# Kernel tuning notes

Hardware: AMD Instinct MI355X
Metric: run time of the kernel (lower is better)

Reference implementation:

```python
import jax, jax.numpy as jnp
import numpy as np

N_U, N_I, D_IN_U, D_IN_I, D, D_QOL, B = 4096, 4096, 256, 256, 256, 4, 8192

def _w(key, shape, scale=0.05):
    return (jax.random.normal(key, shape) * scale).astype(jnp.float32)

def setup_inputs() -> dict:
    key = jax.random.key(0)
    ks = jax.random.split(key, 24)
    inp = {
        "x_u": jax.random.normal(ks[0], (N_U, D_IN_U), jnp.float32),
        "x_i": jax.random.normal(ks[1], (N_I, D_IN_I), jnp.float32),
        "social_adj": jax.random.randint(ks[2], (N_U, N_U), 0, 2, jnp.int32),
        "ui_adj": jax.random.randint(ks[3], (N_U, N_I), 0, 2, jnp.int32),
        "user_idx": jax.random.randint(ks[4], (B,), 0, N_U, jnp.int32),
        "item_idx": jax.random.randint(ks[5], (B,), 0, N_I, jnp.int32),
        "q_u": jax.random.normal(ks[6], (N_U, D_QOL), jnp.float32),
        # params (Linear stored as [in, out]; y = x @ W + b)
        "user_W": _w(ks[7], (D_IN_U, D)), "user_b": jnp.zeros((D,), jnp.float32),
        "item_W": _w(ks[8], (D_IN_I, D)), "item_b": jnp.zeros((D,), jnp.float32),
        "soc_W": _w(ks[9], (D, D)), "soc_a": _w(ks[10], (2 * D,)),
        "cnt_W": _w(ks[11], (D, D)), "cnt_a": _w(ks[12], (2 * D,)),
        "gate_W": _w(ks[13], (D_QOL, D)), "gate_b": jnp.zeros((D,), jnp.float32),
        "qproj_W": _w(ks[14], (D_QOL, D)), "qproj_b": jnp.zeros((D,), jnp.float32),
        "alpha_q": jnp.float32(0.3),
        "pred_W1": _w(ks[15], (2 * D, D)), "pred_b1": jnp.zeros((D,), jnp.float32),
        "pred_W2": _w(ks[16], (D, 1)), "pred_b2": jnp.zeros((1,), jnp.float32),
    }
    return inp

def _gat(Wh_src, Wh_dst, a, adj):
    """GAT additive attention: src rows attend over dst cols where adj!=0.
    Rows with no neighbors produce zero output (matches nan_to_num + zeroing)."""
    d = Wh_src.shape[-1]
    a1 = Wh_src @ a[:d]          # [N_src]
    a2 = Wh_dst @ a[d:]          # [N_dst]
    e = jax.nn.leaky_relu(a1[:, None] + a2[None, :], 0.2)  # [N_src, N_dst]
    mask = adj != 0
    neg_inf = jnp.float32(-jnp.inf)
    m = jnp.max(jnp.where(mask, e, neg_inf), axis=-1, keepdims=True)
    m = jnp.where(jnp.isfinite(m), m, 0.0)  # guard empty rows
    ex = jnp.where(mask, jnp.exp(e - m), 0.0)
    denom = jnp.sum(ex, axis=-1, keepdims=True)
    alpha = jnp.where(denom > 0, ex / jnp.where(denom > 0, denom, 1.0), 0.0)
    out = alpha @ Wh_dst
    return out, alpha

def reference(x_u, x_i, social_adj, ui_adj, user_idx, item_idx, q_u,
              user_W, user_b, item_W, item_b, soc_W, soc_a, cnt_W, cnt_a,
              gate_W, gate_b, qproj_W, qproj_b, alpha_q,
              pred_W1, pred_b1, pred_W2, pred_b2):
    h_u = x_u @ user_W + user_b               # [N_u, D]
    h_i = x_i @ item_W + item_b               # [N_i, D]
    # social attention (users over users)
    Wh = h_u @ soc_W
    soc_msg, alpha_s = _gat(Wh, Wh, soc_a, social_adj)
    # content attention (users over items)
    Wu = h_u @ cnt_W
    Wi = h_i @ cnt_W
    cnt_msg, alpha_c = _gat(Wu, Wi, cnt_a, ui_adj)
    h_u_out = jax.nn.elu(soc_msg + cnt_msg + h_u)
    # QoL gate
    gate = jax.nn.sigmoid(q_u @ gate_W + gate_b)
    qproj = q_u @ qproj_W + qproj_b
    h_u_out = h_u_out + alpha_q * gate * qproj
    # pair prediction (dropout inactive at eval)
    cat = jnp.concatenate([h_u_out[user_idx], h_i[item_idx]], axis=-1)  # [B, 2D]
    hid = jax.nn.relu(cat @ pred_W1 + pred_b1)
    r = (hid @ pred_W2 + pred_b2)[..., 0]
    r_hat = 1.0 + 4.0 * jax.nn.sigmoid(r)
    return r_hat, alpha_s, alpha_c
```

## Files before the change

### kernel.cpp

```cpp
#include <hip/hip_runtime.h>

typedef unsigned short u16;
typedef unsigned int u32;
typedef unsigned char u8;
typedef unsigned long long u64;
typedef float f32x4 __attribute__((ext_vector_type(4)));
typedef __bf16 bf16x8 __attribute__((ext_vector_type(8)));

#define NU 4096
#define DD 256
#define BB 8192

__device__ inline u16 f2b(float f) {
    u32 u = __builtin_bit_cast(u32, f);
    u32 r = (u + 0x7fffu + ((u >> 16) & 1u)) >> 16;
    return (u16)r;
}
__device__ inline float b2f(u16 v) { return __builtin_bit_cast(float, (u32)v << 16); }
__device__ inline float lrelu(float x) { return x > 0.f ? x : 0.2f * x; }
__device__ inline float decmax(u32 e) {
    return __builtin_bit_cast(float, (e >> 31) ? (e & 0x7fffffffu) : ~e);
}

#define BARRIER_LGKM() asm volatile("s_waitcnt lgkmcnt(0)\ns_barrier" ::: "memory")

__global__ __launch_bounds__(256) void k_pro(
    const float* __restrict__ x_u, const float* __restrict__ x_i,
    const float* __restrict__ user_W, const float* __restrict__ item_W, const float* __restrict__ pred_W1,
    const float* __restrict__ soc_W, const float* __restrict__ soc_a,
    const float* __restrict__ cnt_W, const float* __restrict__ cnt_a,
    const float* __restrict__ user_b, const float* __restrict__ item_b,
    u16* __restrict__ xu_b, u16* __restrict__ xi_b,
    u16* __restrict__ uWt, u16* __restrict__ iWt, u16* __restrict__ p1Wt,
    float* __restrict__ uvec,
    u16* __restrict__ WusT, u16* __restrict__ WicT,
    float* __restrict__ b_us, float* __restrict__ b_ic, u32* __restrict__ MhEnc) {
    __shared__ float t[64][65];
    __shared__ float sa[256];
    const int b = blockIdx.x;
    const int tid = threadIdx.x;

    if (b < 1024) {
        const float* in = (b < 512) ? x_u : x_i;
        u16* out = (b < 512) ? xu_b : xi_b;
        int i = (b & 511) * 256 + tid;
        const float4 v0 = *(const float4*)(in + (size_t)i * 8);
        const float4 v1 = *(const float4*)(in + (size_t)i * 8 + 4);
        u16 u[8] = {f2b(v0.x), f2b(v0.y), f2b(v0.z), f2b(v0.w),
                    f2b(v1.x), f2b(v1.y), f2b(v1.z), f2b(v1.w)};
        *(uint4*)(out + (size_t)i * 8) = *(uint4*)u;
    } else if (b < 1088) {
        int j = b - 1024;
        const float* in;
        u16* out;
        int R;
        if (j < 16) { in = user_W; out = uWt; R = 256; }
        else if (j < 32) { in = item_W; out = iWt; R = 256; j -= 16; }
        else { in = pred_W1; out = p1Wt; R = 512; j -= 32; }
        int rb = (j >> 2) * 64, cb = (j & 3) * 64;
        for (int k = 0; k < 16; ++k) {
            int idx = k * 256 + tid;
            int lr = idx >> 6, lc = idx & 63;
            t[lr][lc] = in[(size_t)(rb + lr) * 256 + cb + lc];
        }
        __syncthreads();
        for (int k = 0; k < 16; ++k) {
            int idx = k * 256 + tid;
            int lr = idx >> 6, lc = idx & 63;
            out[(size_t)(cb + lr) * R + rb + lc] = f2b(t[lc][lr]);
        }
    } else if (b < 1092) {
        int bb = b - 1088;
        if (bb == 0 && tid < 2) MhEnc[tid] = 0u;
        const float* W = (bb < 2) ? soc_W : cnt_W;
        const float* a = ((bb < 2) ? soc_a : cnt_a) + (bb & 1) * 256;
        int lane = tid & 63, wv = tid >> 6;
        sa[tid] = a[tid];
        __syncthreads();
        for (int rr = 0; rr < 64; ++rr) {
            int in = wv * 64 + rr;
            float4 w4 = *(const float4*)(W + (size_t)in * 256 + lane * 4);
            float acc = w4.x * sa[lane * 4] + w4.y * sa[lane * 4 + 1] + w4.z * sa[lane * 4 + 2] + w4.w * sa[lane * 4 + 3];
#pragma unroll
            for (int off = 32; off; off >>= 1) acc += __shfl_down(acc, off);
            if (lane == 0) uvec[bb * 256 + in] = acc;
        }
    } else {
        int j = b - 1092;
        int p = j >> 4;
        int tile = j & 15;
        const float* A = p ? item_W : user_W;
        const float* Bw = p ? cnt_W : soc_W;
        const float* bvec = p ? item_b : user_b;
        u16* outT = p ? WicT : WusT;
        float* outb = p ? b_ic : b_us;
        int m0 = (tile >> 2) * 64, n0 = (tile & 3) * 64;
        int m = m0 + (tid >> 4) * 4, n = n0 + (tid & 15) * 4;
        float acc[4][4];
#pragma unroll
        for (int i = 0; i < 4; ++i)
#pragma unroll
            for (int k = 0; k < 4; ++k) acc[i][k] = 0.f;
        for (int k0 = 0; k0 < 256; k0 += 4) {
            float aa[4][4], bb2[4][4];
#pragma unroll
            for (int i = 0; i < 4; ++i) {
                float4 v = *(const float4*)(A + (size_t)(m + i) * 256 + k0);
                aa[i][0] = v.x; aa[i][1] = v.y; aa[i][2] = v.z; aa[i][3] = v.w;
            }
#pragma unroll
            for (int k = 0; k < 4; ++k) {
                float4 v = *(const float4*)(Bw + (size_t)(k0 + k) * 256 + n);
                bb2[k][0] = v.x; bb2[k][1] = v.y; bb2[k][2] = v.z; bb2[k][3] = v.w;
            }
#pragma unroll
            for (int i = 0; i < 4; ++i)
#pragma unroll
                for (int k = 0; k < 4; ++k)
#pragma unroll
                    for (int jj = 0; jj < 4; ++jj) acc[i][jj] += aa[i][k] * bb2[k][jj];
        }
#pragma unroll
        for (int i = 0; i < 4; ++i)
#pragma unroll
            for (int jj = 0; jj < 4; ++jj) outT[(size_t)(n + jj) * 256 + m + i] = f2b(acc[i][jj]);
        if (tile >> 2 == 0 && tid < 64) {
            int nn = n0 + tid;
            float s = 0.f;
            for (int k = 0; k < 256; ++k) s += bvec[k] * Bw[(size_t)k * 256 + nn];
            outb[nn] = s;
        }
    }
}

__global__ __launch_bounds__(256) void k_gemm4(
    const u16* __restrict__ xu_b, const u16* __restrict__ xi_b,
    const u16* __restrict__ uWt, const u16* __restrict__ iWt,
    const u16* __restrict__ WusT, const u16* __restrict__ WicT,
    const float* __restrict__ user_b, const float* __restrict__ item_b,
    const float* __restrict__ b_us, const float* __restrict__ b_ic,
    float* __restrict__ h_u_f, float* __restrict__ h_i_f, u16* __restrict__ h_i_b,
    u16* __restrict__ WhT, u16* __restrict__ WiT) {
    const int z = blockIdx.z;
    const int M = 4096, N = 256, K = 256;
    const u16* A = (z == 0 || z == 2) ? xu_b : xi_b;
    const u16* Bt = (z == 0) ? uWt : (z == 1) ? iWt : (z == 2) ? WusT : WicT;
    const float* bias = (z == 0) ? user_b : (z == 1) ? item_b : (z == 2) ? b_us : b_ic;
    float* Cf = (z == 0) ? h_u_f : (z == 1) ? h_i_f : nullptr;
    u16* Cb = (z == 1) ? h_i_b : nullptr;
    u16* Cbt = (z == 2) ? WhT : (z == 3) ? WiT : nullptr;

    __shared__ u16 As[64 * 64];
    __shared__ u16 Bs[64 * 64];
    const int tid = threadIdx.x;
    const int lane = tid & 63, wv = tid >> 6;
    const int bm = blockIdx.x * 64, bn = blockIdx.y * 64;
    const int wm = (wv >> 1) * 32, wn = (wv & 1) * 32;
    f32x4 acc[2][2];
#pragma unroll
    for (int i = 0; i < 2; i++)
#pragma unroll
        for (int j = 0; j < 2; j++) acc[i][j] = f32x4{0.f, 0.f, 0.f, 0.f};

    char* Ab = (char*)As;
    char* Bb = (char*)Bs;
    const int r = tid >> 2;
    const int ib0 = (tid & 3) * 32;
    const int swz = (r & 7) << 4;

    for (int k0 = 0; k0 < K; k0 += 64) {
        const uint4* ga = (const uint4*)(A + (size_t)(bm + r) * K + k0 + (ib0 >> 1));
        const uint4* gb = (const uint4*)(Bt + (size_t)(bn + r) * K + k0 + (ib0 >> 1));
        uint4 va0 = ga[0], va1 = ga[1];
        uint4 vb0 = gb[0], vb1 = gb[1];
        __syncthreads();
        *(uint4*)(Ab + r * 128 + ((ib0) ^ swz)) = va0;
        *(uint4*)(Ab + r * 128 + ((ib0 + 16) ^ swz)) = va1;
        *(uint4*)(Bb + r * 128 + ((ib0) ^ swz)) = vb0;
        *(uint4*)(Bb + r * 128 + ((ib0 + 16) ^ swz)) = vb1;
        __syncthreads();
#pragma unroll
        for (int kh = 0; kh < 2; ++kh) {
            bf16x8 af[2], bfr[2];
#pragma unroll
            for (int mf = 0; mf < 2; ++mf) {
                int row = wm + mf * 16 + (lane & 15);
                int kb = kh * 64 + ((lane >> 4) << 4);
                af[mf] = *(const bf16x8*)(Ab + row * 128 + (kb ^ ((row & 7) << 4)));
            }
#pragma unroll
            for (int nf = 0; nf < 2; ++nf) {
                int row = wn + nf * 16 + (lane & 15);
                int kb = kh * 64 + ((lane >> 4) << 4);
                bfr[nf] = *(const bf16x8*)(Bb + row * 128 + (kb ^ ((row & 7) << 4)));
            }
#pragma unroll
            for (int mf = 0; mf < 2; ++mf)
#pragma unroll
                for (int nf = 0; nf < 2; ++nf)
                    acc[mf][nf] = __builtin_amdgcn_mfma_f32_16x16x32_bf16(af[mf], bfr[nf], acc[mf][nf], 0, 0, 0);
        }
    }
#pragma unroll
    for (int mf = 0; mf < 2; ++mf) {
#pragma unroll
        for (int nf = 0; nf < 2; ++nf) {
            int col = bn + wn + nf * 16 + (lane & 15);
            int row0 = bm + wm + mf * 16 + ((lane >> 4) << 2);
            float bv = bias[col];
            float v[4];
#pragma unroll
            for (int q = 0; q < 4; ++q) {
                float x = acc[mf][nf][q] + bv;
                v[q] = x;
                if (Cf) Cf[(size_t)(row0 + q) * N + col] = x;
                if (Cb) Cb[(size_t)(row0 + q) * N + col] = f2b(x);
            }
            if (Cbt) {
                uint2 p;
                p.x = (u32)f2b(v[0]) | ((u32)f2b(v[1]) << 16);
                p.y = (u32)f2b(v[2]) | ((u32)f2b(v[3]) << 16);
                *(uint2*)(Cbt + (size_t)col * M + row0) = p;
            }
        }
    }
}

__global__ __launch_bounds__(256) void k_gemv_a(const float* __restrict__ h_u, const float* __restrict__ h_i,
                                                const float* __restrict__ uvec, float* __restrict__ avec,
                                                u32* __restrict__ MhEnc) {
    int tid = threadIdx.x, lane = tid & 63, wv = tid >> 6;
    int ib = blockIdx.x * 64;
    const float* H = (wv == 3) ? h_i : h_u;
    const float* u = uvec + wv * 256;
    float4 u4 = *(const float4*)(u + lane * 4);
    float runm = -1e30f;
    for (int rr = 0; rr < 64; ++rr) {
        int row = ib + rr;
        float4 h4 = *(const float4*)(H + (size_t)row * 256 + lane * 4);
        float acc = h4.x * u4.x + h4.y * u4.y + h4.z * u4.z + h4.w * u4.w;
#pragma unroll
        for (int off = 32; off; off >>= 1) acc += __shfl_down(acc, off);
        if (lane == 0) {
            avec[wv * 4096 + row] = acc;
            runm = fmaxf(runm, acc);
        }
    }
    if (lane == 0 && (wv & 1)) {
        u32 b = __builtin_bit_cast(u32, runm);
        u32 e = (b >> 31) ? ~b : (b | 0x80000000u);
        atomicMax(&MhEnc[wv >> 1], e);
    }
}

__global__ __launch_bounds__(256) void k_scan(const int* __restrict__ adjS, const int* __restrict__ adjC,
                                              u8* __restrict__ bits) {
    const int z = blockIdx.z;
    const int* adj = z ? adjC : adjS;
    u8* bz = bits + (size_t)z * 2097152;
    const int ib = blockIdx.x * 32, jb = blockIdx.y * 512;
    const int lane = threadIdx.x & 63, wv = threadIdx.x >> 6;
    const int r0 = wv * 8;
    const int* base = adj + (size_t)(ib + r0) * 4096 + jb + lane * 8;
    int4 va[8], vb[8];
#pragma unroll
    for (int rr = 0; rr < 8; ++rr) {
        va[rr] = *(const int4*)(base + (size_t)rr * 4096);
        vb[rr] = *(const int4*)(base + (size_t)rr * 4096 + 4);
    }
    const size_t bo = (size_t)(ib + r0) * 512 + (jb >> 3) + lane;
#pragma unroll
    for (int rr = 0; rr < 8; ++rr) {
        int4 v0 = va[rr], v1 = vb[rr];
        u32 b = (u32)(v0.x != 0) | ((u32)(v0.y != 0) << 1) | ((u32)(v0.z != 0) << 2) | ((u32)(v0.w != 0) << 3) |
                ((u32)(v1.x != 0) << 4) | ((u32)(v1.y != 0) << 5) | ((u32)(v1.z != 0) << 6) | ((u32)(v1.w != 0) << 7);
        bz[bo + (size_t)rr * 512] = (u8)b;
    }
}

__global__ __launch_bounds__(512, 4) void k_pv(const u8* __restrict__ bits,
                                               const float* __restrict__ avec, const u32* __restrict__ MhEnc,
                                               const u16* __restrict__ WhT, const u16* __restrict__ WiT,
                                               float* __restrict__ dpart, u16* __restrict__ msgpart) {
    const int z = blockIdx.z;
    const int ib = blockIdx.x * 64;
    const int jb = blockIdx.y * 512;
    const int tid = threadIdx.x, lane = tid & 63, wv = tid >> 6;
    const u8* bz = bits + (size_t)z * 2097152;
    const float* a1 = avec + z * 8192;
    const float* a2 = a1 + 4096;
    const u16* Pt = z ? WiT : WhT;

    __shared__ float a2s[512];
    __shared__ float s_a1[64], s_mr[64];
    __shared__ u16 Atile[64 * 512];
    char* Ab = (char*)Atile;

    if (tid < 512) a2s[tid] = a2[jb + tid];
    if (tid < 64) {
        float a = a1[ib + tid];
        float mhg = decmax(MhEnc[z]);
        s_a1[tid] = a;
        s_mr[tid] = lrelu(a + mhg);
    }
    __syncthreads();

    const int r0 = wv * 8;
    u8 bvv[8];
    const size_t bo = (size_t)(ib + r0) * 512 + (jb >> 3) + lane;
#pragma unroll
    for (int rr = 0; rr < 8; ++rr) bvv[rr] = bz[bo + (size_t)rr * 512];
    const float4 A0 = *(const float4*)(a2s + lane * 8);
    const float4 A1 = *(const float4*)(a2s + lane * 8 + 4);
    const float av[8] = {A0.x, A0.y, A0.z, A0.w, A1.x, A1.y, A1.z, A1.w};
#pragma unroll
    for (int rr = 0; rr < 8; ++rr) {
        const int r = r0 + rr;
        const float a1r = s_a1[r], mr = s_mr[r];
        const u32 byte = bvv[rr];
        float ex[8];
        float acc = 0.f;
#pragma unroll
        for (int k = 0; k < 8; ++k) {
            float e = __expf(lrelu(a1r + av[k]) - mr);
            ex[k] = ((byte >> k) & 1) ? e : 0.f;
            acc += ex[k];
        }
#pragma unroll
        for (int off = 32; off; off >>= 1) acc += __shfl_down(acc, off);
        if (lane == 0) dpart[((size_t)z * 8 + blockIdx.y) * 4096 + ib + r] = acc;
        u16 pk[8];
#pragma unroll
        for (int k = 0; k < 8; ++k) pk[k] = f2b(ex[k]);
        *(uint4*)(Ab + r * 1024 + ((lane * 16) ^ ((r & 7) << 4))) = *(uint4*)pk;
    }
    BARRIER_LGKM();

    f32x4 acc[4][2];
#pragma unroll
    for (int i = 0; i < 4; i++)
#pragma unroll
        for (int j = 0; j < 2; j++) acc[i][j] = f32x4{0.f, 0.f, 0.f, 0.f};

    const u16* pts = Pt + (size_t)(wv * 32 + (lane & 15)) * 4096 + jb + ((lane >> 4) << 3);
    bf16x8 bcur0 = *(const bf16x8*)(pts);
    bf16x8 bcur1 = *(const bf16x8*)(pts + (size_t)16 * 4096);
    for (int ks = 0; ks < 16; ++ks) {
        bf16x8 bnxt0, bnxt1;
        if (ks < 15) {
            bnxt0 = *(const bf16x8*)(pts + (ks + 1) * 32);
            bnxt1 = *(const bf16x8*)(pts + (size_t)16 * 4096 + (ks + 1) * 32);
        }
#pragma unroll
        for (int mf = 0; mf < 4; ++mf) {
            int ra = mf * 16 + (lane & 15);
            bf16x8 af = *(const bf16x8*)(Ab + ra * 1024 + ((ks * 64 + ((lane >> 4) << 4)) ^ ((ra & 7) << 4)));
            acc[mf][0] = __builtin_amdgcn_mfma_f32_16x16x32_bf16(af, bcur0, acc[mf][0], 0, 0, 0);
            acc[mf][1] = __builtin_amdgcn_mfma_f32_16x16x32_bf16(af, bcur1, acc[mf][1], 0, 0, 0);
        }
        bcur0 = bnxt0;
        bcur1 = bnxt1;
    }

    u16* mp = msgpart + ((size_t)(z * 8 + blockIdx.y) * 4096 + ib) * 256;
#pragma unroll
    for (int mf = 0; mf < 4; ++mf) {
        int rr = mf * 16 + ((lane >> 4) << 2);
#pragma unroll
        for (int nf = 0; nf < 2; ++nf) {
            int col = wv * 32 + nf * 16 + (lane & 15);
#pragma unroll
            for (int q = 0; q < 4; ++q) mp[(size_t)(rr + q) * 256 + col] = f2b(acc[mf][nf][q]);
        }
    }
}

__global__ __launch_bounds__(256) void k_alpha(const u8* __restrict__ bits,
                                               const float* __restrict__ avec, const u32* __restrict__ MhEnc,
                                               const float* __restrict__ dpart, float* __restrict__ out) {
    const int z = blockIdx.z;
    const int ib = blockIdx.x * 64;
    const int jb = blockIdx.y * 512;
    const int tid = threadIdx.x, lane = tid & 63, wv = tid >> 6;
    const u8* bz = bits + (size_t)z * 2097152;
    const float* a1 = avec + z * 8192;
    const float* a2 = a1 + 4096;
    float* alpha = out + 8192 + (size_t)z * 16777216;

    __shared__ float s_a1[64], s_mr[64], s_inv[64];
    if (tid < 64) {
        float a = a1[ib + tid];
        float mhg = decmax(MhEnc[z]);
        s_a1[tid] = a;
        s_mr[tid] = lrelu(a + mhg);
        float d = 0.f;
#pragma unroll
        for (int s = 0; s < 8; ++s) d += dpart[((size_t)(z * 8 + s)) * 4096 + ib + tid];
        s_inv[tid] = d > 0.f ? 1.f / d : 0.f;
    }
    const float4 A0 = *(const float4*)(a2 + jb + lane * 4);
    const float4 A1 = *(const float4*)(a2 + jb + 256 + lane * 4);
    const float av0[4] = {A0.x, A0.y, A0.z, A0.w};
    const float av1[4] = {A1.x, A1.y, A1.z, A1.w};
    __syncthreads();

    const int bb0 = (jb >> 3) + (lane >> 1);
    const int sh = (lane & 1) * 4;
    for (int rr = 0; rr < 16; ++rr) {
        const int r = wv * 16 + rr;
        const int row = ib + r;
        const float a1r = s_a1[r], mr = s_mr[r], ivr = s_inv[r];
        const u32 n0 = (u32)(bz[(size_t)row * 512 + bb0]) >> sh;
        const u32 n1 = (u32)(bz[(size_t)row * 512 + bb0 + 32]) >> sh;
        float o0[4], o1[4];
#pragma unroll
        for (int k = 0; k < 4; ++k) {
            o0[k] = ((n0 >> k) & 1) ? __expf(lrelu(a1r + av0[k]) - mr) * ivr : 0.f;
            o1[k] = ((n1 >> k) & 1) ? __expf(lrelu(a1r + av1[k]) - mr) * ivr : 0.f;
        }
        float* ap = alpha + (size_t)row * 4096 + jb;
        *(float4*)(ap + lane * 4) = float4{o0[0], o0[1], o0[2], o0[3]};
        *(float4*)(ap + 256 + lane * 4) = float4{o1[0], o1[1], o1[2], o1[3]};
    }
}

__global__ __launch_bounds__(256) void k_post(const u16* __restrict__ msgpart, const float* __restrict__ dpart,
                                              const float* __restrict__ h_u, const float* __restrict__ q_u,
                                              const float* __restrict__ gate_W, const float* __restrict__ gate_b,
                                              const float* __restrict__ qproj_W, const float* __restrict__ qproj_b,
                                              const float* __restrict__ alpha_q, u16* __restrict__ huo_b) {
    int i = blockIdx.x;
    int n = threadIdx.x;
    __shared__ float red[16];
    if (n < 16) red[n] = dpart[(size_t)n * 4096 + i];
    __syncthreads();
    float d0 = 0.f, d1 = 0.f;
#pragma unroll
    for (int p = 0; p < 8; ++p) { d0 += red[p]; d1 += red[8 + p]; }
    float inv0 = d0 > 0.f ? 1.f / d0 : 0.f;
    float inv1 = d1 > 0.f ? 1.f / d1 : 0.f;
    float s0 = 0.f, s1 = 0.f;
#pragma unroll
    for (int p = 0; p < 8; ++p) {
        s0 += b2f(msgpart[((size_t)p * 4096 + i) * 256 + n]);
        s1 += b2f(msgpart[((size_t)(8 + p) * 4096 + i) * 256 + n]);
    }
    float v = inv0 * s0 + inv1 * s1 + h_u[(size_t)i * 256 + n];
    v = v > 0.f ? v : expm1f(v);
    float q0 = q_u[i * 4 + 0], q1 = q_u[i * 4 + 1], q2 = q_u[i * 4 + 2], q3 = q_u[i * 4 + 3];
    float g = q0 * gate_W[n] + q1 * gate_W[256 + n] + q2 * gate_W[512 + n] + q3 * gate_W[768 + n] + gate_b[n];
    g = 1.f / (1.f + __expf(-g));
    float qp = q0 * qproj_W[n] + q1 * qproj_W[256 + n] + q2 * qproj_W[512 + n] + q3 * qproj_W[768 + n] + qproj_b[n];
    float o = v + alpha_q[0] * g * qp;
    huo_b[(size_t)i * 256 + n] = f2b(o);
}

__global__ __launch_bounds__(512) void k_pred(const u16* __restrict__ huo_b, const u16* __restrict__ h_i_b,
                                              const int* __restrict__ uidx, const int* __restrict__ iidx,
                                              const u16* __restrict__ Bt, const float* __restrict__ b1,
                                              const float* __restrict__ W2, const float* __restrict__ b2,
                                              float* __restrict__ out) {
    __shared__ u16 As[64 * 512];
    __shared__ float redL[512];
    const int tid = threadIdx.x, lane = tid & 63, wv = tid >> 6;
    const int bm = blockIdx.x * 64;
    char* Ab = (char*)As;

    {
        const int r = tid >> 3;
        const int uix = uidx[bm + r], iix = iidx[bm + r];
        const int sswz = (r & 7) << 4;
#pragma unroll
        for (int c = 0; c < 8; ++c) {
            int e = c * 64 + (tid & 7) * 8;
            const u16* src = (e < 256) ? (huo_b + (size_t)uix * 256 + e) : (h_i_b + (size_t)iix * 256 + (e - 256));
            uint4 v = *(const uint4*)src;
            *(uint4*)(Ab + r * 1024 + ((e * 2) ^ sswz)) = v;
        }
    }
    __syncthreads();

    const int n0 = wv * 32;
    f32x4 acc[4][2];
#pragma unroll
    for (int i = 0; i < 4; i++)
#pragma unroll
        for (int j = 0; j < 2; j++) acc[i][j] = f32x4{0.f, 0.f, 0.f, 0.f};

    for (int ks = 0; ks < 16; ++ks) {
        bf16x8 bfr[2];
#pragma unroll
        for (int nf = 0; nf < 2; ++nf)
            bfr[nf] = *(const bf16x8*)(Bt + (size_t)(n0 + nf * 16 + (lane & 15)) * 512 + ks * 32 + ((lane >> 4) << 3));
#pragma unroll
        for (int mf = 0; mf < 4; ++mf) {
            int ra = mf * 16 + (lane & 15);
            bf16x8 af = *(const bf16x8*)(Ab + ra * 1024 + ((ks * 64 + ((lane >> 4) << 4)) ^ ((ra & 7) << 4)));
#pragma unroll
            for (int nf = 0; nf < 2; ++nf)
                acc[mf][nf] = __builtin_amdgcn_mfma_f32_16x16x32_bf16(af, bfr[nf], acc[mf][nf], 0, 0, 0);
        }
    }

    float b1v[2], w2v[2];
#pragma unroll
    for (int nf = 0; nf < 2; ++nf) {
        int col = n0 + nf * 16 + (lane & 15);
        b1v[nf] = b1[col];
        w2v[nf] = W2[col];
    }
#pragma unroll
    for (int mf = 0; mf < 4; ++mf) {
#pragma unroll
        for (int q = 0; q < 4; ++q) {
            float val = 0.f;
#pragma unroll
            for (int nf = 0; nf < 2; ++nf) val += fmaxf(acc[mf][nf][q] + b1v[nf], 0.f) * w2v[nf];
#pragma unroll
            for (int off = 1; off < 16; off <<= 1) val += __shfl_xor(val, off);
            if ((lane & 15) == 0) redL[wv * 64 + mf * 16 + ((lane >> 4) << 2) + q] = val;
        }
    }
    __syncthreads();
    if (tid < 64) {
        float r = b2[0];
#pragma unroll
        for (int w = 0; w < 8; ++w) r += redL[w * 64 + tid];
        out[bm + tid] = 1.f + 4.f / (1.f + __expf(-r));
    }
}

extern "C" void kernel_launch(void* const* d_in, const int* in_sizes, int n_in,
                              void* d_out, int out_size, void* d_ws, size_t ws_size,
                              hipStream_t stream) {
    const float* x_u = (const float*)d_in[0];
    const float* x_i = (const float*)d_in[1];
    const int* adjS = (const int*)d_in[2];
    const int* adjC = (const int*)d_in[3];
    const int* uidx = (const int*)d_in[4];
    const int* iidx = (const int*)d_in[5];
    const float* q_u = (const float*)d_in[6];
    const float* user_W = (const float*)d_in[7];
    const float* user_b = (const float*)d_in[8];
    const float* item_W = (const float*)d_in[9];
    const float* item_b = (const float*)d_in[10];
    const float* soc_W = (const float*)d_in[11];
    const float* soc_a = (const float*)d_in[12];
    const float* cnt_W = (const float*)d_in[13];
    const float* cnt_a = (const float*)d_in[14];
    const float* gate_W = (const float*)d_in[15];
    const float* gate_b = (const float*)d_in[16];
    const float* qproj_W = (const float*)d_in[17];
    const float* qproj_b = (const float*)d_in[18];
    const float* alpha_q = (const float*)d_in[19];
    const float* pred_W1 = (const float*)d_in[20];
    const float* pred_b1 = (const float*)d_in[21];
    const float* pred_W2 = (const float*)d_in[22];
    const float* pred_b2 = (const float*)d_in[23];
    float* out = (float*)d_out;

    char* w = (char*)d_ws;
    size_t off = 0;
    auto alloc = [&](size_t bytes) -> void* {
        void* p = w + off;
        off = (off + bytes + 255) & ~(size_t)255;
        return p;
    };
    u16* xu_b = (u16*)alloc((size_t)NU * DD * 2);
    u16* xi_b = (u16*)alloc((size_t)NU * DD * 2);
    u16* uWt = (u16*)alloc(256 * 256 * 2);
    u16* iWt = (u16*)alloc(256 * 256 * 2);
    u16* p1Wt = (u16*)alloc(512 * 256 * 2);
    u16* WusT = (u16*)alloc(256 * 256 * 2);
    u16* WicT = (u16*)alloc(256 * 256 * 2);
    float* b_us = (float*)alloc(256 * 4);
    float* b_ic = (float*)alloc(256 * 4);
    float* uvec = (float*)alloc(4 * 256 * 4);
    float* h_u_f = (float*)alloc((size_t)NU * DD * 4);
    float* h_i_f = (float*)alloc((size_t)NU * DD * 4);
    u16* h_i_b = (u16*)alloc((size_t)NU * DD * 2);
    u16* WhT = (u16*)alloc((size_t)NU * DD * 2);
    u16* WiT = (u16*)alloc((size_t)NU * DD * 2);
    float* avec = (float*)alloc(4 * 4096 * 4);
    u32* MhEnc = (u32*)alloc(2 * 4);
    float* dpart = (float*)alloc((size_t)2 * 8 * 4096 * 4);
    u8* bits = (u8*)alloc((size_t)2 * 2097152);
    u16* msgpart = (u16*)alloc((size_t)16 * 4096 * 256 * 2);
    u16* huo_b = (u16*)alloc((size_t)NU * DD * 2);
    (void)in_sizes; (void)n_in; (void)out_size; (void)ws_size;

    k_scan<<<dim3(128, 8, 2), 256, 0, stream>>>(adjS, adjC, bits);
    k_pro<<<1124, 256, 0, stream>>>(x_u, x_i, user_W, item_W, pred_W1, soc_W, soc_a, cnt_W, cnt_a,
                                    user_b, item_b, xu_b, xi_b, uWt, iWt, p1Wt, uvec, WusT, WicT,
                                    b_us, b_ic, MhEnc);
    k_gemm4<<<dim3(64, 4, 4), 256, 0, stream>>>(xu_b, xi_b, uWt, iWt, WusT, WicT, user_b, item_b, b_us, b_ic,
                                                h_u_f, h_i_f, h_i_b, WhT, WiT);
    k_gemv_a<<<64, 256, 0, stream>>>(h_u_f, h_i_f, uvec, avec, MhEnc);
    k_pv<<<dim3(64, 8, 2), 512, 0, stream>>>(bits, avec, MhEnc, WhT, WiT, dpart, msgpart);
    k_alpha<<<dim3(64, 8, 2), 256, 0, stream>>>(bits, avec, MhEnc, dpart, out);
    k_post<<<4096, 256, 0, stream>>>(msgpart, dpart, h_u_f, q_u, gate_W, gate_b, qproj_W, qproj_b, alpha_q, huo_b);
    k_pred<<<128, 512, 0, stream>>>(huo_b, h_i_b, uidx, iidx, p1Wt, pred_b1, pred_W2, pred_b2, out);
}
```

Before: 205.5 us.

## Restructure adjacency scan and alpha write kernels for streaming full rows with nontemporal access

k_scan now assigns one full 4096-column adjacency row per wavefront and reads it with nontemporal loads. k_alpha now handles 16 full rows per block: it stages the whole a2 vector and the rows' mask bits in LDS, then writes alpha with nontemporal stores. The goal is to stream the large int32 adjacency reads and the 128MB alpha output more efficiently and avoid polluting cache. The cost is more LDS per k_alpha block (about 24KB), which may lower occupancy.

```diff
diff --git a/kernel.cpp b/kernel.cpp
--- a/kernel.cpp
+++ b/kernel.cpp
@@ -5,6 +5,7 @@
 typedef unsigned char u8;
 typedef unsigned long long u64;
 typedef float f32x4 __attribute__((ext_vector_type(4)));
+typedef int i32x4 __attribute__((ext_vector_type(4)));
 typedef __bf16 bf16x8 __attribute__((ext_vector_type(8)));
 
 #define NU 4096
@@ -253,28 +254,27 @@
     }
 }
 
-__global__ __launch_bounds__(256) void k_scan(const int* __restrict__ adjS, const int* __restrict__ adjC,
+__global__ __launch_bounds__(512) void k_scan(const int* __restrict__ adjS, const int* __restrict__ adjC,
                                               u8* __restrict__ bits) {
     const int z = blockIdx.z;
     const int* adj = z ? adjC : adjS;
     u8* bz = bits + (size_t)z * 2097152;
-    const int ib = blockIdx.x * 32, jb = blockIdx.y * 512;
     const int lane = threadIdx.x & 63, wv = threadIdx.x >> 6;
-    const int r0 = wv * 8;
-    const int* base = adj + (size_t)(ib + r0) * 4096 + jb + lane * 8;
-    int4 va[8], vb[8];
-#pragma unroll
-    for (int rr = 0; rr < 8; ++rr) {
-        va[rr] = *(const int4*)(base + (size_t)rr * 4096);
-        vb[rr] = *(const int4*)(base + (size_t)rr * 4096 + 4);
-    }
-    const size_t bo = (size_t)(ib + r0) * 512 + (jb >> 3) + lane;
-#pragma unroll
-    for (int rr = 0; rr < 8; ++rr) {
-        int4 v0 = va[rr], v1 = vb[rr];
+    const int row = blockIdx.x * 8 + wv;
+    const int* base = adj + (size_t)row * 4096 + lane * 8;
+    i32x4 va[8], vb[8];
+#pragma unroll
+    for (int s = 0; s < 8; ++s) {
+        va[s] = __builtin_nontemporal_load((const i32x4*)(base + s * 512));
+        vb[s] = __builtin_nontemporal_load((const i32x4*)(base + s * 512 + 4));
+    }
+    const size_t bo = (size_t)row * 512 + lane;
+#pragma unroll
+    for (int s = 0; s < 8; ++s) {
+        i32x4 v0 = va[s], v1 = vb[s];
         u32 b = (u32)(v0.x != 0) | ((u32)(v0.y != 0) << 1) | ((u32)(v0.z != 0) << 2) | ((u32)(v0.w != 0) << 3) |
                 ((u32)(v1.x != 0) << 4) | ((u32)(v1.y != 0) << 5) | ((u32)(v1.z != 0) << 6) | ((u32)(v1.w != 0) << 7);
-        bz[bo + (size_t)rr * 512] = (u8)b;
+        bz[bo + s * 64] = (u8)b;
     }
 }
 
@@ -379,16 +379,24 @@
                                                const float* __restrict__ avec, const u32* __restrict__ MhEnc,
                                                const float* __restrict__ dpart, float* __restrict__ out) {
     const int z = blockIdx.z;
-    const int ib = blockIdx.x * 64;
-    const int jb = blockIdx.y * 512;
+    const int ib = blockIdx.x * 16;
     const int tid = threadIdx.x, lane = tid & 63, wv = tid >> 6;
     const u8* bz = bits + (size_t)z * 2097152;
     const float* a1 = avec + z * 8192;
     const float* a2 = a1 + 4096;
     float* alpha = out + 8192 + (size_t)z * 16777216;
 
-    __shared__ float s_a1[64], s_mr[64], s_inv[64];
-    if (tid < 64) {
+    __shared__ float a2s[4096];
+    __shared__ u8 bls[16 * 512];
+    __shared__ float s_a1[16], s_mr[16], s_inv[16];
+
+#pragma unroll
+    for (int k = 0; k < 4; ++k)
+        *(float4*)(a2s + (k * 256 + tid) * 4) = *(const float4*)(a2 + (k * 256 + tid) * 4);
+#pragma unroll
+    for (int k = 0; k < 2; ++k)
+        *(uint4*)(bls + (k * 256 + tid) * 16) = *(const uint4*)(bz + (size_t)ib * 512 + (k * 256 + tid) * 16);
+    if (tid < 16) {
         float a = a1[ib + tid];
         float mhg = decmax(MhEnc[z]);
         s_a1[tid] = a;
@@ -398,29 +406,29 @@
         for (int s = 0; s < 8; ++s) d += dpart[((size_t)(z * 8 + s)) * 4096 + ib + tid];
         s_inv[tid] = d > 0.f ? 1.f / d : 0.f;
     }
-    const float4 A0 = *(const float4*)(a2 + jb + lane * 4);
-    const float4 A1 = *(const float4*)(a2 + jb + 256 + lane * 4);
-    const float av0[4] = {A0.x, A0.y, A0.z, A0.w};
-    const float av1[4] = {A1.x, A1.y, A1.z, A1.w};
     __syncthreads();
 
-    const int bb0 = (jb >> 3) + (lane >> 1);
+    const int bsub = lane >> 1;
     const int sh = (lane & 1) * 4;
-    for (int rr = 0; rr < 16; ++rr) {
-        const int r = wv * 16 + rr;
+#pragma unroll
+    for (int rr = 0; rr < 4; ++rr) {
+        const int r = wv * 4 + rr;
         const int row = ib + r;
         const float a1r = s_a1[r], mr = s_mr[r], ivr = s_inv[r];
-        const u32 n0 = (u32)(bz[(size_t)row * 512 + bb0]) >> sh;
-        const u32 n1 = (u32)(bz[(size_t)row * 512 + bb0 + 32]) >> sh;
-        float o0[4], o1[4];
-#pragma unroll
-        for (int k = 0; k < 4; ++k) {
-            o0[k] = ((n0 >> k) & 1) ? __expf(lrelu(a1r + av0[k]) - mr) * ivr : 0.f;
-            o1[k] = ((n1 >> k) & 1) ? __expf(lrelu(a1r + av1[k]) - mr) * ivr : 0.f;
-        }
-        float* ap = alpha + (size_t)row * 4096 + jb;
-        *(float4*)(ap + lane * 4) = float4{o0[0], o0[1], o0[2], o0[3]};
-        *(float4*)(ap + 256 + lane * 4) = float4{o1[0], o1[1], o1[2], o1[3]};
+        float* ap = alpha + (size_t)row * 4096;
+        const u8* brow = bls + r * 512;
+#pragma unroll
+        for (int c = 0; c < 16; ++c) {
+            const int col = c * 256 + lane * 4;
+            const u32 nib = ((u32)brow[c * 32 + bsub]) >> sh;
+            const float4 a4 = *(const float4*)(a2s + col);
+            f32x4 o;
+            o.x = (nib & 1) ? __expf(lrelu(a1r + a4.x) - mr) * ivr : 0.f;
+            o.y = (nib & 2) ? __expf(lrelu(a1r + a4.y) - mr) * ivr : 0.f;
+            o.z = (nib & 4) ? __expf(lrelu(a1r + a4.z) - mr) * ivr : 0.f;
+            o.w = (nib & 8) ? __expf(lrelu(a1r + a4.w) - mr) * ivr : 0.f;
+            __builtin_nontemporal_store(o, (f32x4*)(ap + col));
+        }
     }
 }
 
@@ -589,7 +597,7 @@
     u16* huo_b = (u16*)alloc((size_t)NU * DD * 2);
     (void)in_sizes; (void)n_in; (void)out_size; (void)ws_size;
 
-    k_scan<<<dim3(128, 8, 2), 256, 0, stream>>>(adjS, adjC, bits);
+    k_scan<<<dim3(512, 1, 2), 512, 0, stream>>>(adjS, adjC, bits);
     k_pro<<<1124, 256, 0, stream>>>(x_u, x_i, user_W, item_W, pred_W1, soc_W, soc_a, cnt_W, cnt_a,
                                     user_b, item_b, xu_b, xi_b, uWt, iWt, p1Wt, uvec, WusT, WicT,
                                     b_us, b_ic, MhEnc);
@@ -597,7 +605,7 @@
                                                 h_u_f, h_i_f, h_i_b, WhT, WiT);
     k_gemv_a<<<64, 256, 0, stream>>>(h_u_f, h_i_f, uvec, avec, MhEnc);
     k_pv<<<dim3(64, 8, 2), 512, 0, stream>>>(bits, avec, MhEnc, WhT, WiT, dpart, msgpart);
-    k_alpha<<<dim3(64, 8, 2), 256, 0, stream>>>(bits, avec, MhEnc, dpart, out);
+    k_alpha<<<dim3(256, 1, 2), 256, 0, stream>>>(bits, avec, MhEnc, dpart, out);
     k_post<<<4096, 256, 0, stream>>>(msgpart, dpart, h_u_f, q_u, gate_W, gate_b, qproj_W, qproj_b, alpha_q, huo_b);
     k_pred<<<128, 512, 0, stream>>>(huo_b, h_i_b, uidx, iidx, p1Wt, pred_b1, pred_W2, pred_b2, out);
 }
```

Result: faster. 192.7 us (-6.2%).
